# Kernel optimization log

Hardware: AMD Instinct MI355X
Metric: run time of the kernel (lower is better)

Reference implementation:

```python
import jax, jax.numpy as jnp
import numpy as np


def _shift(x, n):
    # torch.roll along the last (angular) axis
    return jnp.roll(x, n, axis=3)


def _flip(x, n):
    # mirror about index n along the last axis: out[..., i] = x[..., (n - i) mod W]
    return jnp.roll(jnp.flip(x, axis=3), n + 1, axis=3)


def setup_inputs() -> dict:
    key = jax.random.key(0)
    k1, k2, k3 = jax.random.split(key, 3)
    B, C, H, W = 16, 96, 96, 96
    x = jax.random.normal(k1, (B, C, H, W), dtype=jnp.float32)
    s = jax.random.normal(k2, (B, 5), dtype=jnp.float32)
    w = jax.random.uniform(k3, (B, C, H, W), dtype=jnp.float32) + 0.1  # keep denominator well-conditioned
    return {"x": x, "s": s, "w": w}


def reference(x, s, w):
    # s.shape[1] == 5 branch of SymmetryControl (square symmetry: 3 rotations + 2 mirrors)
    sg = jax.nn.sigmoid(s).reshape(s.shape[0], -1, 1, 1)  # [B,5,1,1]
    step = x.shape[3] // 8

    x90 = _shift(x, step * 2)
    x180 = _shift(x, step * 4)
    x270 = _shift(x, step * 6)
    x90f = _flip(x, step * 2 - 1)
    x180f = _flip(x, step * 4 - 1)

    w90 = sg[:, 0:1] * _shift(w, step * 2)
    w180 = sg[:, 1:2] * _shift(w, step * 4)
    w270 = sg[:, 2:3] * _shift(w, step * 6)
    w90f = sg[:, 3:4] * _flip(w, step * 2 - 1)
    w180f = sg[:, 4:5] * _flip(w, step * 4 - 1)

    a = (w * x + w90 * x90 + w180 * x180 + w270 * x270
         + w90f * x90f + w180f * x180f)
    b = w + w90 + w180 + w270 + w90f + w180f
    return a / b
```

## Files before the change

kernel.cpp:

```cpp
#include <hip/hip_runtime.h>


#define WDIM 96
#define ROWS 16
#define RPB  9216
#define LSTR 100

__global__ __launch_bounds__(24 * ROWS)
void symctl_kernel(const float* __restrict__ x,
                   const float* __restrict__ s,
                   const float* __restrict__ w,
                   float* __restrict__ out) {
    __shared__ float pb[ROWS][LSTR];
    __shared__ float wb[ROWS][LSTR];

    const int t       = threadIdx.x;
    const int ry      = threadIdx.y;
    const int rowbase = blockIdx.x * ROWS;
    const int row     = rowbase + ry;
    const int b       = rowbase / RPB;

    const float* sb = s + b * 5;
    const float sg0 = 1.0f / (1.0f + __expf(-sb[0]));
    const float sg1 = 1.0f / (1.0f + __expf(-sb[1]));
    const float sg2 = 1.0f / (1.0f + __expf(-sb[2]));
    const float sg3 = 1.0f / (1.0f + __expf(-sb[3]));
    const float sg4 = 1.0f / (1.0f + __expf(-sb[4]));

    const float4 x4 = ((const float4*)(x + (size_t)row * WDIM))[t];
    const float4 w4 = ((const float4*)(w + (size_t)row * WDIM))[t];
    float4 p4;
    p4.x = x4.x * w4.x; p4.y = x4.y * w4.y;
    p4.z = x4.z * w4.z; p4.w = x4.w * w4.w;
    *(float4*)&pb[ry][4 * t] = p4;
    *(float4*)&wb[ry][4 * t] = w4;

    __syncthreads();

    const int r  = t;
    const int rm = 23 - t;
    const float* pr = &pb[ry][0];
    const float* wr = &wb[ry][0];

    float pq[4], aq[4], pP[4], aP[4];
#pragma unroll
    for (int q = 0; q < 4; ++q) {
        pq[q] = pr[24 * q + r];
        aq[q] = wr[24 * q + r];
        pP[q] = pr[24 * q + rm];
        aP[q] = wr[24 * q + rm];
    }

    float* orow = out + (size_t)row * WDIM + r;
#pragma unroll
    for (int q = 0; q < 4; ++q) {
        const int i1 = (q + 3) & 3;
        const int i2 = (q + 2) & 3;
        const int i3 = (q + 1) & 3;
        const int i4 = (4 - q) & 3;
        const int i5 = (5 - q) & 3;

        float num = pq[q];
        num = fmaf(sg0, pq[i1], num);
        num = fmaf(sg1, pq[i2], num);
        num = fmaf(sg2, pq[i3], num);
        num = fmaf(sg3, pP[i4], num);
        num = fmaf(sg4, pP[i5], num);

        float den = aq[q];
        den = fmaf(sg0, aq[i1], den);
        den = fmaf(sg1, aq[i2], den);
        den = fmaf(sg2, aq[i3], den);
        den = fmaf(sg3, aP[i4], den);
        den = fmaf(sg4, aP[i5], den);

        orow[24 * q] = num * __builtin_amdgcn_rcpf(den);
    }
}

extern "C" void kernel_launch(void* const* d_in, const int* in_sizes, int n_in,
                              void* d_out, int out_size, void* d_ws, size_t ws_size,
                              hipStream_t stream) {
    const float* x = (const float*)d_in[0];
    const float* s = (const float*)d_in[1];
    const float* w = (const float*)d_in[2];
    float* out = (float*)d_out;

    const int n_rows = in_sizes[0] / WDIM;
    const int grid = n_rows / ROWS;

    dim3 block(24, ROWS);
    symctl_kernel<<<grid, block, 0, stream>>>(x, s, w, out);
}
```

Before: 149.6 us.

## Make kernel persistent with double-buffered LDS and register prefetch of next tile

Converts the one-tile-per-block kernel into a grid-strided persistent loop capped at a fixed grid size. The next tile's x and w loads are issued into registers before the current tile is processed, and shared memory is double-buffered so only one barrier per iteration is needed. The goal is to overlap global loads with compute and cut block launch overhead. This adds LDS use and a hand-written waitcnt/barrier, which lowers occupancy and may reduce memory-level parallelism for a purely bandwidth-bound kernel.

```diff
diff --git a/kernel.cpp b/kernel.cpp
--- a/kernel.cpp
+++ b/kernel.cpp
@@ -4,78 +4,103 @@
 #define WDIM 96
 #define ROWS 16
 #define RPB  9216
-#define LSTR 100
+#define LSTR 120
+#define GRID 2304
 
 __global__ __launch_bounds__(24 * ROWS)
 void symctl_kernel(const float* __restrict__ x,
                    const float* __restrict__ s,
                    const float* __restrict__ w,
-                   float* __restrict__ out) {
-    __shared__ float pb[ROWS][LSTR];
-    __shared__ float wb[ROWS][LSTR];
+                   float* __restrict__ out,
+                   int ntiles) {
+    __shared__ float pb[2][ROWS][LSTR];
+    __shared__ float wb[2][ROWS][LSTR];
 
-    const int t       = threadIdx.x;
-    const int ry      = threadIdx.y;
-    const int rowbase = blockIdx.x * ROWS;
-    const int row     = rowbase + ry;
-    const int b       = rowbase / RPB;
+    const int t  = threadIdx.x;
+    const int ry = threadIdx.y;
+    const int gstride = gridDim.x;
 
-    const float* sb = s + b * 5;
-    const float sg0 = 1.0f / (1.0f + __expf(-sb[0]));
-    const float sg1 = 1.0f / (1.0f + __expf(-sb[1]));
-    const float sg2 = 1.0f / (1.0f + __expf(-sb[2]));
-    const float sg3 = 1.0f / (1.0f + __expf(-sb[3]));
-    const float sg4 = 1.0f / (1.0f + __expf(-sb[4]));
+    int tile = blockIdx.x;
 
-    const float4 x4 = ((const float4*)(x + (size_t)row * WDIM))[t];
-    const float4 w4 = ((const float4*)(w + (size_t)row * WDIM))[t];
-    float4 p4;
-    p4.x = x4.x * w4.x; p4.y = x4.y * w4.y;
-    p4.z = x4.z * w4.z; p4.w = x4.w * w4.w;
-    *(float4*)&pb[ry][4 * t] = p4;
-    *(float4*)&wb[ry][4 * t] = w4;
+    {
+        const size_t row = (size_t)tile * ROWS + ry;
+    }
+    const size_t row0 = (size_t)tile * ROWS + ry;
+    float4 xa = ((const float4*)(x + row0 * WDIM))[t];
+    float4 wa = ((const float4*)(w + row0 * WDIM))[t];
 
-    __syncthreads();
+    int buf = 0;
+    bool more = true;
+    do {
+        const int cur = tile;
 
-    const int r  = t;
-    const int rm = 23 - t;
-    const float* pr = &pb[ry][0];
-    const float* wr = &wb[ry][0];
+        float4 p4;
+        p4.x = xa.x * wa.x; p4.y = xa.y * wa.y;
+        p4.z = xa.z * wa.z; p4.w = xa.w * wa.w;
+        *(float4*)&pb[buf][ry][4 * t] = p4;
+        *(float4*)&wb[buf][ry][4 * t] = wa;
 
-    float pq[4], aq[4], pP[4], aP[4];
+        tile += gstride;
+        more = (tile < ntiles);
+        if (more) {
+            const size_t nrow = (size_t)tile * ROWS + ry;
+            xa = ((const float4*)(x + nrow * WDIM))[t];
+            wa = ((const float4*)(w + nrow * WDIM))[t];
+        }
+
+        const int b = (cur * ROWS) / RPB;
+        const float* sb = s + b * 5;
+        const float sg0 = 1.0f / (1.0f + __expf(-sb[0]));
+        const float sg1 = 1.0f / (1.0f + __expf(-sb[1]));
+        const float sg2 = 1.0f / (1.0f + __expf(-sb[2]));
+        const float sg3 = 1.0f / (1.0f + __expf(-sb[3]));
+        const float sg4 = 1.0f / (1.0f + __expf(-sb[4]));
+
+        asm volatile("s_waitcnt lgkmcnt(0)" ::: "memory");
+        __builtin_amdgcn_s_barrier();
+
+        const int r  = t;
+        const int rm = 23 - t;
+        const float* pr = &pb[buf][ry][0];
+        const float* wr = &wb[buf][ry][0];
+
+        float pq[4], aq[4], pP[4], aP[4];
 #pragma unroll
-    for (int q = 0; q < 4; ++q) {
-        pq[q] = pr[24 * q + r];
-        aq[q] = wr[24 * q + r];
-        pP[q] = pr[24 * q + rm];
-        aP[q] = wr[24 * q + rm];
-    }
+        for (int q = 0; q < 4; ++q) {
+            pq[q] = pr[24 * q + r];
+            aq[q] = wr[24 * q + r];
+            pP[q] = pr[24 * q + rm];
+            aP[q] = wr[24 * q + rm];
+        }
 
-    float* orow = out + (size_t)row * WDIM + r;
+        float* orow = out + (size_t)((size_t)cur * ROWS + ry) * WDIM + r;
 #pragma unroll
-    for (int q = 0; q < 4; ++q) {
-        const int i1 = (q + 3) & 3;
-        const int i2 = (q + 2) & 3;
-        const int i3 = (q + 1) & 3;
-        const int i4 = (4 - q) & 3;
-        const int i5 = (5 - q) & 3;
+        for (int q = 0; q < 4; ++q) {
+            const int i1 = (q + 3) & 3;
+            const int i2 = (q + 2) & 3;
+            const int i3 = (q + 1) & 3;
+            const int i4 = (4 - q) & 3;
+            const int i5 = (5 - q) & 3;
 
-        float num = pq[q];
-        num = fmaf(sg0, pq[i1], num);
-        num = fmaf(sg1, pq[i2], num);
-        num = fmaf(sg2, pq[i3], num);
-        num = fmaf(sg3, pP[i4], num);
-        num = fmaf(sg4, pP[i5], num);
+            float num = pq[q];
+            num = fmaf(sg0, pq[i1], num);
+            num = fmaf(sg1, pq[i2], num);
+            num = fmaf(sg2, pq[i3], num);
+            num = fmaf(sg3, pP[i4], num);
+            num = fmaf(sg4, pP[i5], num);
 
-        float den = aq[q];
-        den = fmaf(sg0, aq[i1], den);
-        den = fmaf(sg1, aq[i2], den);
-        den = fmaf(sg2, aq[i3], den);
-        den = fmaf(sg3, aP[i4], den);
-        den = fmaf(sg4, aP[i5], den);
+            float den = aq[q];
+            den = fmaf(sg0, aq[i1], den);
+            den = fmaf(sg1, aq[i2], den);
+            den = fmaf(sg2, aq[i3], den);
+            den = fmaf(sg3, aP[i4], den);
+            den = fmaf(sg4, aP[i5], den);
 
-        orow[24 * q] = num * __builtin_amdgcn_rcpf(den);
-    }
+            orow[24 * q] = num * __builtin_amdgcn_rcpf(den);
+        }
+
+        buf ^= 1;
+    } while (more);
 }
 
 extern "C" void kernel_launch(void* const* d_in, const int* in_sizes, int n_in,
@@ -86,9 +111,12 @@
     const float* w = (const float*)d_in[2];
     float* out = (float*)d_out;
 
-    const int n_rows = in_sizes[0] / WDIM;
-    const int grid = n_rows / ROWS;
+    const int n_rows = in_sizes[0] / (WDIM * 4);
+    const int n_rows_elems = in_sizes[0] / WDIM;
+    const int ntiles = n_rows_elems / ROWS;
+
+    const int grid = (ntiles < GRID) ? ntiles : GRID;
 
     dim3 block(24, ROWS);
-    symctl_kernel<<<grid, block, 0, stream>>>(x, s, w, out);
+    symctl_kernel<<<grid, block, 0, stream>>>(x, s, w, out, ntiles);
 }
```

Measured after the change: 154.9 us. +3.6%, slower.

## Replace LDS staging with wave-level bpermute shuffles in persistent grid-stride loop

Applied to the files above, without the earlier changes.

Each wave now handles two rows per iteration (32 lanes per row, 3 contiguous floats per lane) and gathers rotated and mirrored neighbours with ds_bpermute instead of staging through shared memory behind a block barrier. A persistent grid of fixed size walks row pairs, prefetching the next pair's x and w into registers and recomputing the sigmoids only when the batch index changes. This removes __syncthreads and LDS round trips, but adds 30 bpermute operations per iteration and uses float3 accesses, which are less wide than the previous float4 loads.

```diff
diff --git a/kernel.cpp b/kernel.cpp
--- a/kernel.cpp
+++ b/kernel.cpp
@@ -2,79 +2,115 @@
 
 
 #define WDIM 96
-#define ROWS 16
 #define RPB  9216
-#define LSTR 100
+#define QPB  (RPB / 2)
+#define WPB  4
+#define GRID 2048
 
-__global__ __launch_bounds__(24 * ROWS)
+__device__ __forceinline__ float bperm(int byteidx, float v) {
+    return __int_as_float(__builtin_amdgcn_ds_bpermute(byteidx, __float_as_int(v)));
+}
+
+__global__ __launch_bounds__(64 * WPB)
 void symctl_kernel(const float* __restrict__ x,
                    const float* __restrict__ s,
                    const float* __restrict__ w,
-                   float* __restrict__ out) {
-    __shared__ float pb[ROWS][LSTR];
-    __shared__ float wb[ROWS][LSTR];
+                   float* __restrict__ out,
+                   int total_q) {
+    const int lane = threadIdx.x & 63;
+    const int tl   = lane & 31;
+    const int hsel = lane & 32;
+    const int h    = lane >> 5;
 
-    const int t       = threadIdx.x;
-    const int ry      = threadIdx.y;
-    const int rowbase = blockIdx.x * ROWS;
-    const int row     = rowbase + ry;
-    const int b       = rowbase / RPB;
+    const int gw = blockIdx.x * WPB + (threadIdx.x >> 6);
+    const int nw = gridDim.x * WPB;
 
-    const float* sb = s + b * 5;
-    const float sg0 = 1.0f / (1.0f + __expf(-sb[0]));
-    const float sg1 = 1.0f / (1.0f + __expf(-sb[1]));
-    const float sg2 = 1.0f / (1.0f + __expf(-sb[2]));
-    const float sg3 = 1.0f / (1.0f + __expf(-sb[3]));
-    const float sg4 = 1.0f / (1.0f + __expf(-sb[4]));
+    const int span = (total_q + nw - 1) / nw;
+    const int q0 = gw * span;
+    const int q1 = min(q0 + span, total_q);
+    if (q0 >= q1) return;
 
-    const float4 x4 = ((const float4*)(x + (size_t)row * WDIM))[t];
-    const float4 w4 = ((const float4*)(w + (size_t)row * WDIM))[t];
-    float4 p4;
-    p4.x = x4.x * w4.x; p4.y = x4.y * w4.y;
-    p4.z = x4.z * w4.z; p4.w = x4.w * w4.w;
-    *(float4*)&pb[ry][4 * t] = p4;
-    *(float4*)&wb[ry][4 * t] = w4;
+    const int i90  = (hsel | ((tl -  8) & 31)) << 2;
+    const int i180 = (hsel | ((tl - 16) & 31)) << 2;
+    const int i270 = (hsel | ((tl +  8) & 31)) << 2;
+    const int f90  = (hsel | (( 7 - tl) & 31)) << 2;
+    const int f180 = (hsel | ((15 - tl) & 31)) << 2;
 
-    __syncthreads();
+    int bcur = -1;
+    float sg0 = 0.f, sg1 = 0.f, sg2 = 0.f, sg3 = 0.f, sg4 = 0.f;
 
-    const int r  = t;
-    const int rm = 23 - t;
-    const float* pr = &pb[ry][0];
-    const float* wr = &wb[ry][0];
+    size_t off = (size_t)(2 * q0 + h) * WDIM + 3 * tl;
+    float3 xv = *(const float3*)(x + off);
+    float3 wv = *(const float3*)(w + off);
 
-    float pq[4], aq[4], pP[4], aP[4];
-#pragma unroll
-    for (int q = 0; q < 4; ++q) {
-        pq[q] = pr[24 * q + r];
-        aq[q] = wr[24 * q + r];
-        pP[q] = pr[24 * q + rm];
-        aP[q] = wr[24 * q + rm];
-    }
+    for (int q = q0; q < q1; ++q) {
+        const float3 xc = xv;
+        const float3 wc = wv;
 
-    float* orow = out + (size_t)row * WDIM + r;
-#pragma unroll
-    for (int q = 0; q < 4; ++q) {
-        const int i1 = (q + 3) & 3;
-        const int i2 = (q + 2) & 3;
-        const int i3 = (q + 1) & 3;
-        const int i4 = (4 - q) & 3;
-        const int i5 = (5 - q) & 3;
+        if (q + 1 < q1) {
+            const size_t noff = (size_t)(2 * (q + 1) + h) * WDIM + 3 * tl;
+            xv = *(const float3*)(x + noff);
+            wv = *(const float3*)(w + noff);
+        }
 
-        float num = pq[q];
-        num = fmaf(sg0, pq[i1], num);
-        num = fmaf(sg1, pq[i2], num);
-        num = fmaf(sg2, pq[i3], num);
-        num = fmaf(sg3, pP[i4], num);
-        num = fmaf(sg4, pP[i5], num);
+        const int b = q / QPB;
+        if (b != bcur) {
+            bcur = b;
+            const float* sb = s + b * 5;
+            sg0 = 1.0f / (1.0f + __expf(-sb[0]));
+            sg1 = 1.0f / (1.0f + __expf(-sb[1]));
+            sg2 = 1.0f / (1.0f + __expf(-sb[2]));
+            sg3 = 1.0f / (1.0f + __expf(-sb[3]));
+            sg4 = 1.0f / (1.0f + __expf(-sb[4]));
+        }
 
-        float den = aq[q];
-        den = fmaf(sg0, aq[i1], den);
-        den = fmaf(sg1, aq[i2], den);
-        den = fmaf(sg2, aq[i3], den);
-        den = fmaf(sg3, aP[i4], den);
-        den = fmaf(sg4, aP[i5], den);
+        const float p0 = xc.x * wc.x;
+        const float p1 = xc.y * wc.y;
+        const float p2 = xc.z * wc.z;
 
-        orow[24 * q] = num * __builtin_amdgcn_rcpf(den);
+        float n0 = p0,   n1 = p1,   n2 = p2;
+        float d0 = wc.x, d1 = wc.y, d2 = wc.z;
+
+        n0 = fmaf(sg0, bperm(i90,  p0),   n0);
+        n1 = fmaf(sg0, bperm(i90,  p1),   n1);
+        n2 = fmaf(sg0, bperm(i90,  p2),   n2);
+        d0 = fmaf(sg0, bperm(i90,  wc.x), d0);
+        d1 = fmaf(sg0, bperm(i90,  wc.y), d1);
+        d2 = fmaf(sg0, bperm(i90,  wc.z), d2);
+
+        n0 = fmaf(sg1, bperm(i180, p0),   n0);
+        n1 = fmaf(sg1, bperm(i180, p1),   n1);
+        n2 = fmaf(sg1, bperm(i180, p2),   n2);
+        d0 = fmaf(sg1, bperm(i180, wc.x), d0);
+        d1 = fmaf(sg1, bperm(i180, wc.y), d1);
+        d2 = fmaf(sg1, bperm(i180, wc.z), d2);
+
+        n0 = fmaf(sg2, bperm(i270, p0),   n0);
+        n1 = fmaf(sg2, bperm(i270, p1),   n1);
+        n2 = fmaf(sg2, bperm(i270, p2),   n2);
+        d0 = fmaf(sg2, bperm(i270, wc.x), d0);
+        d1 = fmaf(sg2, bperm(i270, wc.y), d1);
+        d2 = fmaf(sg2, bperm(i270, wc.z), d2);
+
+        n0 = fmaf(sg3, bperm(f90,  p2),   n0);
+        n1 = fmaf(sg3, bperm(f90,  p1),   n1);
+        n2 = fmaf(sg3, bperm(f90,  p0),   n2);
+        d0 = fmaf(sg3, bperm(f90,  wc.z), d0);
+        d1 = fmaf(sg3, bperm(f90,  wc.y), d1);
+        d2 = fmaf(sg3, bperm(f90,  wc.x), d2);
+
+        n0 = fmaf(sg4, bperm(f180, p2),   n0);
+        n1 = fmaf(sg4, bperm(f180, p1),   n1);
+        n2 = fmaf(sg4, bperm(f180, p0),   n2);
+        d0 = fmaf(sg4, bperm(f180, wc.z), d0);
+        d1 = fmaf(sg4, bperm(f180, wc.y), d1);
+        d2 = fmaf(sg4, bperm(f180, wc.x), d2);
+
+        float3 o;
+        o.x = n0 * __builtin_amdgcn_rcpf(d0);
+        o.y = n1 * __builtin_amdgcn_rcpf(d1);
+        o.z = n2 * __builtin_amdgcn_rcpf(d2);
+        *(float3*)(out + (size_t)(2 * q + h) * WDIM + 3 * tl) = o;
     }
 }
 
@@ -86,9 +122,13 @@
     const float* w = (const float*)d_in[2];
     float* out = (float*)d_out;
 
-    const int n_rows = in_sizes[0] / WDIM;
-    const int grid = n_rows / ROWS;
+    const int n_rows  = in_sizes[0] / WDIM;
+    const int total_q = n_rows / 2;
 
-    dim3 block(24, ROWS);
-    symctl_kernel<<<grid, block, 0, stream>>>(x, s, w, out);
+    const int waves_needed = total_q;
+    int grid = GRID;
+    if (grid * WPB > waves_needed) grid = (waves_needed + WPB - 1) / WPB;
+
+    dim3 block(64 * WPB);
+    symctl_kernel<<<grid, block, 0, stream>>>(x, s, w, out, total_q);
 }
```

Result: slower. 158.7 us (+6.1%).

## Pipeline multi-tile blocks with async global-to-LDS loads

Applied to the files above, without the earlier changes.

Each block now handles 12 tiles of 16 rows instead of one. Tiles are staged through a 4-deep LDS ring buffer filled by the `global_load_lds` builtin, with manual `vmcnt` waits and barriers, so the loads for later tiles overlap compute and stores on the current tile. The x*w product now happens after the LDS read rather than before the write. The aim is to hide memory latency and cut per-block launch overhead in this bandwidth-bound kernel, at the cost of more LDS per block, fewer blocks and hand-written wait counts.

```diff
diff --git a/kernel.cpp b/kernel.cpp
--- a/kernel.cpp
+++ b/kernel.cpp
@@ -3,23 +3,44 @@
 
 #define WDIM 96
 #define ROWS 16
-#define RPB  9216
-#define LSTR 100
+#define TILE_FLOATS (ROWS * WDIM)
+#define DD 4
+#define T_TILES 12
+#define RPB 9216
 
-__global__ __launch_bounds__(24 * ROWS)
+__device__ __forceinline__ void g2l16(const float* g, float* l) {
+    __builtin_amdgcn_global_load_lds(
+        (const __attribute__((address_space(1))) void*)g,
+        (__attribute__((address_space(3))) void*)l,
+        16, 0, 0);
+}
+
+__global__ __launch_bounds__(384)
 void symctl_kernel(const float* __restrict__ x,
                    const float* __restrict__ s,
                    const float* __restrict__ w,
                    float* __restrict__ out) {
-    __shared__ float pb[ROWS][LSTR];
-    __shared__ float wb[ROWS][LSTR];
+    __shared__ float xb[DD][TILE_FLOATS];
+    __shared__ float wb[DD][TILE_FLOATS];
 
-    const int t       = threadIdx.x;
-    const int ry      = threadIdx.y;
-    const int rowbase = blockIdx.x * ROWS;
-    const int row     = rowbase + ry;
-    const int b       = rowbase / RPB;
+    const int tid  = threadIdx.x;
+    const int wv   = tid >> 6;
+    const int lane = tid & 63;
 
+    const int chunk = wv * 256 + lane * 4;
+    const float* ldsx_base = &xb[0][0] + wv * 256;
+    const float* ldsw_base = &wb[0][0] + wv * 256;
+
+    const int tile0 = blockIdx.x * T_TILES;
+
+#pragma unroll
+    for (int d = 0; d < DD - 1; ++d) {
+        const size_t gbase = (size_t)(tile0 + d) * TILE_FLOATS + chunk;
+        g2l16(x + gbase, (float*)(ldsx_base + d * TILE_FLOATS));
+        g2l16(w + gbase, (float*)(ldsw_base + d * TILE_FLOATS));
+    }
+
+    const int b = (tile0 * ROWS) / RPB;
     const float* sb = s + b * 5;
     const float sg0 = 1.0f / (1.0f + __expf(-sb[0]));
     const float sg1 = 1.0f / (1.0f + __expf(-sb[1]));
@@ -27,54 +48,65 @@
     const float sg3 = 1.0f / (1.0f + __expf(-sb[3]));
     const float sg4 = 1.0f / (1.0f + __expf(-sb[4]));
 
-    const float4 x4 = ((const float4*)(x + (size_t)row * WDIM))[t];
-    const float4 w4 = ((const float4*)(w + (size_t)row * WDIM))[t];
-    float4 p4;
-    p4.x = x4.x * w4.x; p4.y = x4.y * w4.y;
-    p4.z = x4.z * w4.z; p4.w = x4.w * w4.w;
-    *(float4*)&pb[ry][4 * t] = p4;
-    *(float4*)&wb[ry][4 * t] = w4;
+    const int t24 = tid % 24;
+    const int ry  = tid / 24;
+    const int r   = t24;
+    const int rm  = 23 - t24;
 
-    __syncthreads();
+    for (int t = 0; t < T_TILES; ++t) {
+        const int d = t & (DD - 1);
 
-    const int r  = t;
-    const int rm = 23 - t;
-    const float* pr = &pb[ry][0];
-    const float* wr = &wb[ry][0];
+        if (t < T_TILES - 2)       asm volatile("s_waitcnt vmcnt(4)" ::: "memory");
+        else if (t == T_TILES - 2) asm volatile("s_waitcnt vmcnt(2)" ::: "memory");
+        else                       asm volatile("s_waitcnt vmcnt(0)" ::: "memory");
+        __builtin_amdgcn_s_barrier();
 
-    float pq[4], aq[4], pP[4], aP[4];
+        if (t + DD - 1 < T_TILES) {
+            const int dn = (t + DD - 1) & (DD - 1);
+            const size_t gbase = (size_t)(tile0 + t + DD - 1) * TILE_FLOATS + chunk;
+            g2l16(x + gbase, (float*)(ldsx_base + dn * TILE_FLOATS));
+            g2l16(w + gbase, (float*)(ldsw_base + dn * TILE_FLOATS));
+        }
+
+        const float* xr = &xb[d][ry * WDIM];
+        const float* wr = &wb[d][ry * WDIM];
+
+        float pq[4], aq[4], pP[4], aP[4];
 #pragma unroll
-    for (int q = 0; q < 4; ++q) {
-        pq[q] = pr[24 * q + r];
-        aq[q] = wr[24 * q + r];
-        pP[q] = pr[24 * q + rm];
-        aP[q] = wr[24 * q + rm];
-    }
+        for (int q = 0; q < 4; ++q) {
+            const float xq = xr[24 * q + r];
+            const float wq = wr[24 * q + r];
+            const float xm = xr[24 * q + rm];
+            const float wm = wr[24 * q + rm];
+            pq[q] = xq * wq;  aq[q] = wq;
+            pP[q] = xm * wm;  aP[q] = wm;
+        }
 
-    float* orow = out + (size_t)row * WDIM + r;
+        float* orow = out + (size_t)((tile0 + t) * ROWS + ry) * WDIM + r;
 #pragma unroll
-    for (int q = 0; q < 4; ++q) {
-        const int i1 = (q + 3) & 3;
-        const int i2 = (q + 2) & 3;
-        const int i3 = (q + 1) & 3;
-        const int i4 = (4 - q) & 3;
-        const int i5 = (5 - q) & 3;
+        for (int q = 0; q < 4; ++q) {
+            const int i1 = (q + 3) & 3;
+            const int i2 = (q + 2) & 3;
+            const int i3 = (q + 1) & 3;
+            const int i4 = (4 - q) & 3;
+            const int i5 = (5 - q) & 3;
 
-        float num = pq[q];
-        num = fmaf(sg0, pq[i1], num);
-        num = fmaf(sg1, pq[i2], num);
-        num = fmaf(sg2, pq[i3], num);
-        num = fmaf(sg3, pP[i4], num);
-        num = fmaf(sg4, pP[i5], num);
+            float num = pq[q];
+            num = fmaf(sg0, pq[i1], num);
+            num = fmaf(sg1, pq[i2], num);
+            num = fmaf(sg2, pq[i3], num);
+            num = fmaf(sg3, pP[i4], num);
+            num = fmaf(sg4, pP[i5], num);
 
-        float den = aq[q];
-        den = fmaf(sg0, aq[i1], den);
-        den = fmaf(sg1, aq[i2], den);
-        den = fmaf(sg2, aq[i3], den);
-        den = fmaf(sg3, aP[i4], den);
-        den = fmaf(sg4, aP[i5], den);
+            float den = aq[q];
+            den = fmaf(sg0, aq[i1], den);
+            den = fmaf(sg1, aq[i2], den);
+            den = fmaf(sg2, aq[i3], den);
+            den = fmaf(sg3, aP[i4], den);
+            den = fmaf(sg4, aP[i5], den);
 
-        orow[24 * q] = num * __builtin_amdgcn_rcpf(den);
+            orow[24 * q] = num * __builtin_amdgcn_rcpf(den);
+        }
     }
 }
 
@@ -87,8 +119,8 @@
     float* out = (float*)d_out;
 
     const int n_rows = in_sizes[0] / WDIM;
-    const int grid = n_rows / ROWS;
+    const int grid   = n_rows / (ROWS * T_TILES);
 
-    dim3 block(24, ROWS);
+    dim3 block(384);
     symctl_kernel<<<grid, block, 0, stream>>>(x, s, w, out);
 }
```

Measured after the change: 160.0 us. 6.9% more time.
